# Performance work log

Measured on AMD Instinct MI355X. Metric: run time of the kernel, lower is better.

## Reference

```python
import jax, jax.numpy as jnp
import numpy as np

P = 8192  # num_particles
C = 8192  # num EEG channels (must equal P for the original broadcast to be valid)


def setup_inputs() -> dict:
    key = jax.random.key(0)
    k1, k2, k3, k4, k5 = jax.random.split(key, 5)
    inputs = jax.random.normal(k1, (1, C, P), dtype=jnp.float32)
    state_vector = jax.random.normal(k2, (P, 3), dtype=jnp.float32)
    # near-identity transition for numerical sanity
    transition_matrix = jnp.eye(3, dtype=jnp.float32) + 0.01 * jax.random.normal(k3, (3, 3), dtype=jnp.float32)
    # symmetric positive-definite process noise covariance (Cholesky must succeed)
    a = jax.random.normal(k4, (3, 3), dtype=jnp.float32)
    process_noise_cov = 0.01 * (a @ a.T) + 0.1 * jnp.eye(3, dtype=jnp.float32)
    forward_matrix = jax.random.normal(k5, (C, 3), dtype=jnp.float32)
    return {
        "inputs": inputs,
        "state_vector": state_vector,
        "transition_matrix": transition_matrix,
        "process_noise_cov": process_noise_cov,
        "forward_matrix": forward_matrix,
    }


def reference(inputs, state_vector, transition_matrix, process_noise_cov, forward_matrix):
    k_noise, k_cat = jax.random.split(jax.random.key(42))
    # --- state transition: x_new = x @ T^T + eps,  eps ~ N(0, Q) via z @ chol(Q) ---
    updated = state_vector @ transition_matrix.T                      # (P, 3)
    L = jnp.linalg.cholesky(process_noise_cov)                        # (3, 3) lower
    z = jax.random.normal(k_noise, (P, 3), dtype=state_vector.dtype)
    state = updated + z @ L                                           # (P, 3)
    # --- EEG measurement model: H @ x^T -> (C, P) ---
    predicted = forward_matrix @ state.T                              # (C, P)
    # --- particle weights: squared-residual sum (broadcast (1,C,P) - (P,C), C==P) ---
    w = jnp.sum(jnp.square(inputs - predicted.T), axis=-1)[0]         # (P,)
    # --- categorical resampling on log-weights (unnormalized logits) ---
    idx = jax.random.categorical(k_cat, jnp.log(w), shape=(P,))       # (P,) int
    resampled = state[idx]                                            # (P, 3) gather
    return jnp.mean(resampled, axis=0)                                # (3,)
```

## Files before the change

kernel.cpp:

```cpp
#include <hip/hip_runtime.h>
#include <stdint.h>

#define NP 8192
#define NC 8192

__host__ __device__ inline uint32_t rotl32(uint32_t x, int r) {
  return __builtin_rotateleft32(x, (unsigned)r);
}

__host__ __device__ inline void threefry2x32(uint32_t k0, uint32_t k1,
                                             uint32_t x0, uint32_t x1,
                                             uint32_t& o0, uint32_t& o1) {
  uint32_t ks2 = k0 ^ k1 ^ 0x1BD11BDAu;
  x0 += k0; x1 += k1;
#define TF_R(r) { x0 += x1; x1 = rotl32(x1, (r)); x1 ^= x0; }
  TF_R(13) TF_R(15) TF_R(26) TF_R(6)   x0 += k1;  x1 += ks2 + 1u;
  TF_R(17) TF_R(29) TF_R(16) TF_R(24)  x0 += ks2; x1 += k0 + 2u;
  TF_R(13) TF_R(15) TF_R(26) TF_R(6)   x0 += k0;  x1 += k1 + 3u;
  TF_R(17) TF_R(29) TF_R(16) TF_R(24)  x0 += k1;  x1 += ks2 + 4u;
  TF_R(13) TF_R(15) TF_R(26) TF_R(6)   x0 += ks2; x1 += k0 + 5u;
#undef TF_R
  o0 = x0; o1 = x1;
}

__device__ inline uint32_t tf_bits(uint32_t k0, uint32_t k1, uint32_t i) {
  uint32_t o0, o1;
  threefry2x32(k0, k1, 0u, i, o0, o1);
  return o0 ^ o1;
}

__device__ inline float u01(uint32_t bits) {
  return __uint_as_float((bits >> 9) | 0x3f800000u) - 1.0f;
}

__device__ inline float egen(uint32_t k0, uint32_t k1, uint32_t ctr) {
  const float TINY = 1.17549435e-38f;
  uint32_t bits = tf_bits(k0, k1, ctr);
  float v = fmaxf(u01(bits), TINY);
  return -__logf(v);
}

__device__ inline float erfinvf_(float x) {
  float w = -log1pf(-x * x);
  float p;
  if (w < 5.0f) {
    w -= 2.5f;
    p = 2.81022636e-08f;
    p = fmaf(p, w, 3.43273939e-07f);
    p = fmaf(p, w, -3.5233877e-06f);
    p = fmaf(p, w, -4.39150654e-06f);
    p = fmaf(p, w, 0.00021858087f);
    p = fmaf(p, w, -0.00125372503f);
    p = fmaf(p, w, -0.00417768164f);
    p = fmaf(p, w, 0.246640727f);
    p = fmaf(p, w, 1.50140941f);
  } else {
    w = sqrtf(w) - 3.0f;
    p = -0.000200214257f;
    p = fmaf(p, w, 0.000100950558f);
    p = fmaf(p, w, 0.00134934322f);
    p = fmaf(p, w, -0.00367342844f);
    p = fmaf(p, w, 0.00573950773f);
    p = fmaf(p, w, -0.0076224613f);
    p = fmaf(p, w, 0.00943887047f);
    p = fmaf(p, w, 1.00167406f);
    p = fmaf(p, w, 2.83297682f);
  }
  return p * x;
}

__global__ void __launch_bounds__(256) k_prep(uint32_t k0, uint32_t k1,
                                              const float* __restrict__ sv,
                                              const float* __restrict__ T,
                                              const float* __restrict__ Q,
                                              const float* __restrict__ H,
                                              float* __restrict__ st,
                                              float* __restrict__ ht) {
  int b = blockIdx.x;
  if (b < 32) {
    int i = b * 256 + threadIdx.x;
    const float lo = -0.99999994f;
    float zz[3];
#pragma unroll
    for (int k = 0; k < 3; k++) {
      uint32_t bits = tf_bits(k0, k1, 3u * (uint32_t)i + (uint32_t)k);
      float v = fmaxf(lo, u01(bits) * 2.0f + lo);
      zz[k] = 1.41421356f * erfinvf_(v);
    }
    float L00 = sqrtf(Q[0]);
    float L10 = Q[3] / L00, L20 = Q[6] / L00;
    float L11 = sqrtf(Q[4] - L10 * L10);
    float L21 = (Q[7] - L20 * L10) / L11;
    float L22 = sqrtf(Q[8] - L20 * L20 - L21 * L21);
    float s0 = sv[i * 3], s1 = sv[i * 3 + 1], s2 = sv[i * 3 + 2];
    float u0 = s0 * T[0] + s1 * T[1] + s2 * T[2];
    float u1 = s0 * T[3] + s1 * T[4] + s2 * T[5];
    float u2 = s0 * T[6] + s1 * T[7] + s2 * T[8];
    st[i * 3]     = u0 + (zz[0] * L00 + zz[1] * L10 + zz[2] * L20);
    st[i * 3 + 1] = u1 + (zz[1] * L11 + zz[2] * L21);
    st[i * 3 + 2] = u2 + (zz[2] * L22);
  } else {
    int t = (b - 32) * 256 + threadIdx.x;
    int k = t >> 13, j = t & (NP - 1);
    ht[t] = H[j * 3 + k];
  }
}

__global__ void __launch_bounds__(256) k_fused(uint32_t k0, uint32_t k1,
                                               const float* __restrict__ in,
                                               const float* __restrict__ ht,
                                               const float* __restrict__ st,
                                               float* __restrict__ winv,
                                               float* __restrict__ E) {
  int b = blockIdx.x;
  if (b % 5 == 0) {
    int w = b / 5;
    int wave = threadIdx.x >> 6;
    int lane = threadIdx.x & 63;
    int row = w * 4 + wave;
    float s0 = st[row * 3], s1 = st[row * 3 + 1], s2 = st[row * 3 + 2];
    const float4* inrow = (const float4*)(in + (size_t)row * NC);
    const float4* h0 = (const float4*)ht;
    const float4* h1 = (const float4*)(ht + NC);
    const float4* h2 = (const float4*)(ht + 2 * NC);
    float acc = 0.0f;
#pragma unroll 4
    for (int it = lane; it < NC / 4; it += 64) {
      float4 x = inrow[it];
      float4 a = h0[it];
      float4 bb = h1[it];
      float4 c = h2[it];
      float d0 = x.x - (a.x * s0 + bb.x * s1 + c.x * s2);
      float d1 = x.y - (a.y * s0 + bb.y * s1 + c.y * s2);
      float d2 = x.z - (a.z * s0 + bb.z * s1 + c.z * s2);
      float d3 = x.w - (a.w * s0 + bb.w * s1 + c.w * s2);
      acc += d0 * d0 + d1 * d1 + d2 * d2 + d3 * d3;
    }
#pragma unroll
    for (int off = 32; off > 0; off >>= 1) acc += __shfl_down(acc, off, 64);
    if (lane == 0) winv[row] = 1.0f / acc;
  } else {
    int s = b - b / 5 - 1;
    uint32_t base = (uint32_t)s * (uint32_t)NP;
    float4* erow = (float4*)(E + (size_t)s * NP);
#pragma unroll 2
    for (int p = 0; p < 8; ++p) {
      uint32_t i0 = (uint32_t)(p * 1024 + 4 * threadIdx.x);
      float4 e;
      e.x = egen(k0, k1, base + i0);
      e.y = egen(k0, k1, base + i0 + 1u);
      e.z = egen(k0, k1, base + i0 + 2u);
      e.w = egen(k0, k1, base + i0 + 3u);
      erow[i0 >> 2] = e;
    }
  }
}

__global__ void __launch_bounds__(256) k_race(const float* __restrict__ E,
                                              const float* __restrict__ winv,
                                              int* __restrict__ idx) {
  int wave = threadIdx.x >> 6;
  int lane = threadIdx.x & 63;
  int s = blockIdx.x * 4 + wave;
  const float4* erow = (const float4*)(E + (size_t)s * NP);
  const float4* wv = (const float4*)winv;
  float best = 3.4e38f;
  int bi = 0;
#pragma unroll 4
  for (int it = lane; it < NP / 4; it += 64) {
    float4 e = erow[it];
    float4 w = wv[it];
    int i = it * 4;
    float r0 = e.x * w.x;
    float r1 = e.y * w.y;
    float r2 = e.z * w.z;
    float r3 = e.w * w.w;
    if (r0 < best) { best = r0; bi = i; }
    if (r1 < best) { best = r1; bi = i + 1; }
    if (r2 < best) { best = r2; bi = i + 2; }
    if (r3 < best) { best = r3; bi = i + 3; }
  }
#pragma unroll
  for (int off = 32; off > 0; off >>= 1) {
    float ob = __shfl_down(best, off, 64);
    int oi = __shfl_down(bi, off, 64);
    if (ob < best || (ob == best && oi < bi)) { best = ob; bi = oi; }
  }
  if (lane == 0) idx[s] = bi;
}

__global__ void __launch_bounds__(256) k_weights(const float* __restrict__ in,
                                                 const float* __restrict__ ht,
                                                 const float* __restrict__ st,
                                                 float* __restrict__ winv) {
  int wave = threadIdx.x >> 6;
  int lane = threadIdx.x & 63;
  int row = blockIdx.x * 4 + wave;
  float s0 = st[row * 3], s1 = st[row * 3 + 1], s2 = st[row * 3 + 2];
  const float4* inrow = (const float4*)(in + (size_t)row * NC);
  const float4* h0 = (const float4*)ht;
  const float4* h1 = (const float4*)(ht + NC);
  const float4* h2 = (const float4*)(ht + 2 * NC);
  float acc = 0.0f;
#pragma unroll 4
  for (int it = lane; it < NC / 4; it += 64) {
    float4 x = inrow[it];
    float4 a = h0[it];
    float4 b = h1[it];
    float4 c = h2[it];
    float d0 = x.x - (a.x * s0 + b.x * s1 + c.x * s2);
    float d1 = x.y - (a.y * s0 + b.y * s1 + c.y * s2);
    float d2 = x.z - (a.z * s0 + b.z * s1 + c.z * s2);
    float d3 = x.w - (a.w * s0 + b.w * s1 + c.w * s2);
    acc += d0 * d0 + d1 * d1 + d2 * d2 + d3 * d3;
  }
#pragma unroll
  for (int off = 32; off > 0; off >>= 1) acc += __shfl_down(acc, off, 64);
  if (lane == 0) winv[row] = 1.0f / acc;
}

__global__ void __launch_bounds__(256) k_resample(uint32_t k0, uint32_t k1,
                                                  const float* __restrict__ winv,
                                                  int* __restrict__ idx) {
  uint32_t s = blockIdx.x;
  uint32_t base = s * (uint32_t)NP;
  const float TINY = 1.17549435e-38f;
  float best = 3.4e38f;
  int bi = 0;
#pragma unroll 4
  for (uint32_t i = threadIdx.x; i < NP; i += 256) {
    uint32_t bits = tf_bits(k0, k1, base + i);
    float v = fmaxf(u01(bits), TINY);
    float r = -__logf(v) * winv[i];
    if (r < best) { best = r; bi = (int)i; }
  }
  __shared__ float rv[256];
  __shared__ int ri[256];
  rv[threadIdx.x] = best;
  ri[threadIdx.x] = bi;
  __syncthreads();
  for (int stp = 128; stp > 0; stp >>= 1) {
    if (threadIdx.x < stp) {
      float va = rv[threadIdx.x], vb = rv[threadIdx.x + stp];
      int ia = ri[threadIdx.x], ib = ri[threadIdx.x + stp];
      if (vb < va || (vb == va && ib < ia)) { rv[threadIdx.x] = vb; ri[threadIdx.x] = ib; }
    }
    __syncthreads();
  }
  if (threadIdx.x == 0) idx[s] = ri[0];
}

__global__ void __launch_bounds__(1024) k_mean(const float* __restrict__ st,
                                               const int* __restrict__ idx,
                                               float* __restrict__ out) {
  double a0 = 0, a1 = 0, a2 = 0;
  for (int s = threadIdx.x; s < NP; s += 1024) {
    int j = idx[s];
    a0 += st[j * 3];
    a1 += st[j * 3 + 1];
    a2 += st[j * 3 + 2];
  }
  __shared__ double r0[1024], r1[1024], r2[1024];
  r0[threadIdx.x] = a0; r1[threadIdx.x] = a1; r2[threadIdx.x] = a2;
  __syncthreads();
  for (int s = 512; s > 0; s >>= 1) {
    if (threadIdx.x < s) {
      r0[threadIdx.x] += r0[threadIdx.x + s];
      r1[threadIdx.x] += r1[threadIdx.x + s];
      r2[threadIdx.x] += r2[threadIdx.x + s];
    }
    __syncthreads();
  }
  if (threadIdx.x == 0) {
    out[0] = (float)(r0[0] / NP);
    out[1] = (float)(r1[0] / NP);
    out[2] = (float)(r2[0] / NP);
  }
}

extern "C" void kernel_launch(void* const* d_in, const int* in_sizes, int n_in,
                              void* d_out, int out_size, void* d_ws, size_t ws_size,
                              hipStream_t stream) {
  const float* in = (const float*)d_in[0];
  const float* sv = (const float*)d_in[1];
  const float* T  = (const float*)d_in[2];
  const float* Q  = (const float*)d_in[3];
  const float* H  = (const float*)d_in[4];
  float* out = (float*)d_out;

  uint32_t nk0, nk1, ck0, ck1;
  threefry2x32(0u, 42u, 0u, 0u, nk0, nk1);
  threefry2x32(0u, 42u, 0u, 1u, ck0, ck1);

  const size_t eFloats = (size_t)NP * (size_t)NP;
  const size_t tailBytes = (24576 + 24576 + NP + NP) * 4;
  const bool fused = ws_size >= eFloats * 4 + tailBytes;

  if (fused) {
    float* E    = (float*)d_ws;
    float* st   = E + eFloats;
    float* ht   = st + 24576;
    float* winv = ht + 24576;
    int*   idx  = (int*)(winv + NP);

    hipLaunchKernelGGL(k_prep, dim3(128), dim3(256), 0, stream, nk0, nk1, sv, T, Q, H, st, ht);
    hipLaunchKernelGGL(k_fused, dim3(10240), dim3(256), 0, stream, ck0, ck1, in, ht, st, winv, E);
    hipLaunchKernelGGL(k_race, dim3(NP / 4), dim3(256), 0, stream, E, winv, idx);
    hipLaunchKernelGGL(k_mean, dim3(1), dim3(1024), 0, stream, st, idx, out);
  } else {
    float* st   = (float*)d_ws;
    float* ht   = st + 24576;
    float* winv = ht + 24576;
    int*   idx  = (int*)(winv + NP);

    hipLaunchKernelGGL(k_prep, dim3(128), dim3(256), 0, stream, nk0, nk1, sv, T, Q, H, st, ht);
    hipLaunchKernelGGL(k_weights, dim3(NP / 4), dim3(256), 0, stream, in, ht, st, winv);
    hipLaunchKernelGGL(k_resample, dim3(NP), dim3(256), 0, stream, ck0, ck1, winv, idx);
    hipLaunchKernelGGL(k_mean, dim3(1), dim3(1024), 0, stream, st, idx, out);
  }
}
```

Measured before the change: 527.9 us.

## Let noise blocks finish the resampling race early once all weights are ready

The fused kernel is rebalanced so weight blocks come first (two weight blocks per noise block in the first 3072 blocks). A global atomic counter records how many weight blocks have completed. A noise block that sees all weights done computes its argmin directly from registers and marks a flag, which skips writing its 256MB share of the E matrix. The race kernel then skips rows whose flag is set. This avoids E write and read traffic for late rows, at the cost of atomics, fences and extra register pressure from holding 32 noise values per thread.

```diff
diff --git a/kernel.cpp b/kernel.cpp
--- a/kernel.cpp
+++ b/kernel.cpp
@@ -3,6 +3,7 @@
 
 #define NP 8192
 #define NC 8192
+#define NWBLK 2048
 
 __host__ __device__ inline uint32_t rotl32(uint32_t x, int r) {
   return __builtin_rotateleft32(x, (unsigned)r);
@@ -75,7 +76,9 @@
                                               const float* __restrict__ Q,
                                               const float* __restrict__ H,
                                               float* __restrict__ st,
-                                              float* __restrict__ ht) {
+                                              float* __restrict__ ht,
+                                              int* __restrict__ flag,
+                                              int* __restrict__ ctrs) {
   int b = blockIdx.x;
   if (b < 32) {
     int i = b * 256 + threadIdx.x;
@@ -99,10 +102,14 @@
     st[i * 3]     = u0 + (zz[0] * L00 + zz[1] * L10 + zz[2] * L20);
     st[i * 3 + 1] = u1 + (zz[1] * L11 + zz[2] * L21);
     st[i * 3 + 2] = u2 + (zz[2] * L22);
-  } else {
+  } else if (b < 128) {
     int t = (b - 32) * 256 + threadIdx.x;
     int k = t >> 13, j = t & (NP - 1);
     ht[t] = H[j * 3 + k];
+  } else {
+    int t = (b - 128) * 256 + threadIdx.x;
+    flag[t] = 0;
+    if (b == 128 && threadIdx.x < 2) ctrs[threadIdx.x] = 0;
   }
 }
 
@@ -111,10 +118,14 @@
                                                const float* __restrict__ ht,
                                                const float* __restrict__ st,
                                                float* __restrict__ winv,
-                                               float* __restrict__ E) {
+                                               float* __restrict__ E,
+                                               int* __restrict__ flag,
+                                               int* __restrict__ idx,
+                                               int* __restrict__ ctrs) {
   int b = blockIdx.x;
-  if (b % 5 == 0) {
-    int w = b / 5;
+  bool isW = (b < 3072) && ((b % 3) < 2);
+  if (isW) {
+    int w = (b / 3) * 2 + (b % 3);
     int wave = threadIdx.x >> 6;
     int lane = threadIdx.x & 63;
     int row = w * 4 + wave;
@@ -139,29 +150,85 @@
 #pragma unroll
     for (int off = 32; off > 0; off >>= 1) acc += __shfl_down(acc, off, 64);
     if (lane == 0) winv[row] = 1.0f / acc;
+    __syncthreads();
+    if (threadIdx.x == 0) {
+      __threadfence();
+      __hip_atomic_fetch_add(&ctrs[0], 1, __ATOMIC_RELEASE, __HIP_MEMORY_SCOPE_AGENT);
+    }
   } else {
-    int s = b - b / 5 - 1;
+    int s = (b < 3072) ? (b / 3) : (1024 + (b - 3072));
     uint32_t base = (uint32_t)s * (uint32_t)NP;
-    float4* erow = (float4*)(E + (size_t)s * NP);
-#pragma unroll 2
+    float e[32];
+#pragma unroll
     for (int p = 0; p < 8; ++p) {
       uint32_t i0 = (uint32_t)(p * 1024 + 4 * threadIdx.x);
-      float4 e;
-      e.x = egen(k0, k1, base + i0);
-      e.y = egen(k0, k1, base + i0 + 1u);
-      e.z = egen(k0, k1, base + i0 + 2u);
-      e.w = egen(k0, k1, base + i0 + 3u);
-      erow[i0 >> 2] = e;
+      e[4 * p + 0] = egen(k0, k1, base + i0);
+      e[4 * p + 1] = egen(k0, k1, base + i0 + 1u);
+      e[4 * p + 2] = egen(k0, k1, base + i0 + 2u);
+      e[4 * p + 3] = egen(k0, k1, base + i0 + 3u);
+    }
+    __shared__ int rdy;
+    if (threadIdx.x == 0) {
+      rdy = (__hip_atomic_load(&ctrs[0], __ATOMIC_ACQUIRE,
+                               __HIP_MEMORY_SCOPE_AGENT) == NWBLK);
+    }
+    __syncthreads();
+    if (rdy) {
+      const float4* wv = (const float4*)winv;
+      float best = 3.4e38f;
+      int bi = 0;
+#pragma unroll
+      for (int p = 0; p < 8; ++p) {
+        uint32_t i0 = (uint32_t)(p * 1024 + 4 * threadIdx.x);
+        float4 w4 = wv[i0 >> 2];
+        float r0 = e[4 * p + 0] * w4.x;
+        float r1 = e[4 * p + 1] * w4.y;
+        float r2 = e[4 * p + 2] * w4.z;
+        float r3 = e[4 * p + 3] * w4.w;
+        int i = (int)i0;
+        if (r0 < best) { best = r0; bi = i; }
+        if (r1 < best) { best = r1; bi = i + 1; }
+        if (r2 < best) { best = r2; bi = i + 2; }
+        if (r3 < best) { best = r3; bi = i + 3; }
+      }
+      __shared__ float rv[256];
+      __shared__ int ri[256];
+      rv[threadIdx.x] = best;
+      ri[threadIdx.x] = bi;
+      __syncthreads();
+      for (int stp = 128; stp > 0; stp >>= 1) {
+        if (threadIdx.x < stp) {
+          float va = rv[threadIdx.x], vb = rv[threadIdx.x + stp];
+          int ia = ri[threadIdx.x], ib = ri[threadIdx.x + stp];
+          if (vb < va || (vb == va && ib < ia)) { rv[threadIdx.x] = vb; ri[threadIdx.x] = ib; }
+        }
+        __syncthreads();
+      }
+      if (threadIdx.x == 0) { idx[s] = ri[0]; flag[s] = 1; }
+    } else {
+      float4* erow = (float4*)(E + (size_t)s * NP);
+#pragma unroll
+      for (int p = 0; p < 8; ++p) {
+        uint32_t i0 = (uint32_t)(p * 1024 + 4 * threadIdx.x);
+        float4 e4;
+        e4.x = e[4 * p + 0];
+        e4.y = e[4 * p + 1];
+        e4.z = e[4 * p + 2];
+        e4.w = e[4 * p + 3];
+        erow[i0 >> 2] = e4;
+      }
     }
   }
 }
 
 __global__ void __launch_bounds__(256) k_race(const float* __restrict__ E,
                                               const float* __restrict__ winv,
+                                              const int* __restrict__ flag,
                                               int* __restrict__ idx) {
   int wave = threadIdx.x >> 6;
   int lane = threadIdx.x & 63;
   int s = blockIdx.x * 4 + wave;
+  if (flag[s]) return;
   const float4* erow = (const float4*)(E + (size_t)s * NP);
   const float4* wv = (const float4*)winv;
   float best = 3.4e38f;
@@ -187,6 +254,34 @@
     if (ob < best || (ob == best && oi < bi)) { best = ob; bi = oi; }
   }
   if (lane == 0) idx[s] = bi;
+}
+
+__global__ void __launch_bounds__(1024) k_mean(const float* __restrict__ st,
+                                               const int* __restrict__ idx,
+                                               float* __restrict__ out) {
+  double a0 = 0, a1 = 0, a2 = 0;
+  for (int s = threadIdx.x; s < NP; s += 1024) {
+    int j = idx[s];
+    a0 += st[j * 3];
+    a1 += st[j * 3 + 1];
+    a2 += st[j * 3 + 2];
+  }
+  __shared__ double r0[1024], r1[1024], r2[1024];
+  r0[threadIdx.x] = a0; r1[threadIdx.x] = a1; r2[threadIdx.x] = a2;
+  __syncthreads();
+  for (int s = 512; s > 0; s >>= 1) {
+    if (threadIdx.x < s) {
+      r0[threadIdx.x] += r0[threadIdx.x + s];
+      r1[threadIdx.x] += r1[threadIdx.x + s];
+      r2[threadIdx.x] += r2[threadIdx.x + s];
+    }
+    __syncthreads();
+  }
+  if (threadIdx.x == 0) {
+    out[0] = (float)(r0[0] / NP);
+    out[1] = (float)(r1[0] / NP);
+    out[2] = (float)(r2[0] / NP);
+  }
 }
 
 __global__ void __launch_bounds__(256) k_weights(const float* __restrict__ in,
@@ -250,34 +345,6 @@
   if (threadIdx.x == 0) idx[s] = ri[0];
 }
 
-__global__ void __launch_bounds__(1024) k_mean(const float* __restrict__ st,
-                                               const int* __restrict__ idx,
-                                               float* __restrict__ out) {
-  double a0 = 0, a1 = 0, a2 = 0;
-  for (int s = threadIdx.x; s < NP; s += 1024) {
-    int j = idx[s];
-    a0 += st[j * 3];
-    a1 += st[j * 3 + 1];
-    a2 += st[j * 3 + 2];
-  }
-  __shared__ double r0[1024], r1[1024], r2[1024];
-  r0[threadIdx.x] = a0; r1[threadIdx.x] = a1; r2[threadIdx.x] = a2;
-  __syncthreads();
-  for (int s = 512; s > 0; s >>= 1) {
-    if (threadIdx.x < s) {
-      r0[threadIdx.x] += r0[threadIdx.x + s];
-      r1[threadIdx.x] += r1[threadIdx.x + s];
-      r2[threadIdx.x] += r2[threadIdx.x + s];
-    }
-    __syncthreads();
-  }
-  if (threadIdx.x == 0) {
-    out[0] = (float)(r0[0] / NP);
-    out[1] = (float)(r1[0] / NP);
-    out[2] = (float)(r2[0] / NP);
-  }
-}
-
 extern "C" void kernel_launch(void* const* d_in, const int* in_sizes, int n_in,
                               void* d_out, int out_size, void* d_ws, size_t ws_size,
                               hipStream_t stream) {
@@ -293,7 +360,7 @@
   threefry2x32(0u, 42u, 0u, 1u, ck0, ck1);
 
   const size_t eFloats = (size_t)NP * (size_t)NP;
-  const size_t tailBytes = (24576 + 24576 + NP + NP) * 4;
+  const size_t tailBytes = (24576 + 24576 + NP + NP + NP + 2) * 4;
   const bool fused = ws_size >= eFloats * 4 + tailBytes;
 
   if (fused) {
@@ -302,10 +369,12 @@
     float* ht   = st + 24576;
     float* winv = ht + 24576;
     int*   idx  = (int*)(winv + NP);
-
-    hipLaunchKernelGGL(k_prep, dim3(128), dim3(256), 0, stream, nk0, nk1, sv, T, Q, H, st, ht);
-    hipLaunchKernelGGL(k_fused, dim3(10240), dim3(256), 0, stream, ck0, ck1, in, ht, st, winv, E);
-    hipLaunchKernelGGL(k_race, dim3(NP / 4), dim3(256), 0, stream, E, winv, idx);
+    int*   flag = idx + NP;
+    int*   ctrs = flag + NP;
+
+    hipLaunchKernelGGL(k_prep, dim3(160), dim3(256), 0, stream, nk0, nk1, sv, T, Q, H, st, ht, flag, ctrs);
+    hipLaunchKernelGGL(k_fused, dim3(10240), dim3(256), 0, stream, ck0, ck1, in, ht, st, winv, E, flag, idx, ctrs);
+    hipLaunchKernelGGL(k_race, dim3(NP / 4), dim3(256), 0, stream, E, winv, flag, idx);
     hipLaunchKernelGGL(k_mean, dim3(1), dim3(1024), 0, stream, st, idx, out);
   } else {
     float* st   = (float*)d_ws;
@@ -313,7 +382,7 @@
     float* winv = ht + 24576;
     int*   idx  = (int*)(winv + NP);
 
-    hipLaunchKernelGGL(k_prep, dim3(128), dim3(256), 0, stream, nk0, nk1, sv, T, Q, H, st, ht);
+    hipLaunchKernelGGL(k_prep, dim3(128), dim3(256), 0, stream, nk0, nk1, sv, T, Q, H, st, ht, (int*)nullptr, (int*)nullptr);
     hipLaunchKernelGGL(k_weights, dim3(NP / 4), dim3(256), 0, stream, in, ht, st, winv);
     hipLaunchKernelGGL(k_resample, dim3(NP), dim3(256), 0, stream, ck0, ck1, winv, idx);
     hipLaunchKernelGGL(k_mean, dim3(1), dim3(1024), 0, stream, st, idx, out);
```

Result: slower. 753.8 us (+42.8%).

## Split random-draw work between fused pass and race kernel

Applied to the files above, without the earlier changes.

The fused pass now precomputes only 6144 of the 8192 rows of categorical noise, interleaved with the weight computation in a 1:3 block pattern. The race kernel mixes blocks that scan stored noise rows with blocks that regenerate the remaining 2048 rows on the fly and race them against the weights. This rebalances RNG compute against the memory traffic of storing and reloading the noise matrix, so compute-bound and bandwidth-bound work overlap better. The cost is a more complex block mapping, and the on-the-fly blocks run heavier threefry and log work in the final pass.

```diff
diff --git a/kernel.cpp b/kernel.cpp
--- a/kernel.cpp
+++ b/kernel.cpp
@@ -3,6 +3,8 @@
 
 #define NP 8192
 #define NC 8192
+#define NS_E 6144
+#define NS_D 2048
 
 __host__ __device__ inline uint32_t rotl32(uint32_t x, int r) {
   return __builtin_rotateleft32(x, (unsigned)r);
@@ -113,8 +115,8 @@
                                                float* __restrict__ winv,
                                                float* __restrict__ E) {
   int b = blockIdx.x;
-  if (b % 5 == 0) {
-    int w = b / 5;
+  if ((b & 3) == 0) {
+    int w = b >> 2;
     int wave = threadIdx.x >> 6;
     int lane = threadIdx.x & 63;
     int row = w * 4 + wave;
@@ -140,7 +142,7 @@
     for (int off = 32; off > 0; off >>= 1) acc += __shfl_down(acc, off, 64);
     if (lane == 0) winv[row] = 1.0f / acc;
   } else {
-    int s = b - b / 5 - 1;
+    int s = b - (b >> 2) - 1;
     uint32_t base = (uint32_t)s * (uint32_t)NP;
     float4* erow = (float4*)(E + (size_t)s * NP);
 #pragma unroll 2
@@ -156,37 +158,98 @@
   }
 }
 
-__global__ void __launch_bounds__(256) k_race(const float* __restrict__ E,
+__global__ void __launch_bounds__(256) k_race(uint32_t k0, uint32_t k1,
+                                              const float* __restrict__ E,
                                               const float* __restrict__ winv,
                                               int* __restrict__ idx) {
-  int wave = threadIdx.x >> 6;
-  int lane = threadIdx.x & 63;
-  int s = blockIdx.x * 4 + wave;
-  const float4* erow = (const float4*)(E + (size_t)s * NP);
-  const float4* wv = (const float4*)winv;
-  float best = 3.4e38f;
-  int bi = 0;
-#pragma unroll 4
-  for (int it = lane; it < NP / 4; it += 64) {
-    float4 e = erow[it];
-    float4 w = wv[it];
-    int i = it * 4;
-    float r0 = e.x * w.x;
-    float r1 = e.y * w.y;
-    float r2 = e.z * w.z;
-    float r3 = e.w * w.w;
-    if (r0 < best) { best = r0; bi = i; }
-    if (r1 < best) { best = r1; bi = i + 1; }
-    if (r2 < best) { best = r2; bi = i + 2; }
-    if (r3 < best) { best = r3; bi = i + 3; }
-  }
+  int b = blockIdx.x;
+  int m = b % 7;
+  if (m < 3) {
+    int e = (b / 7) * 3 + m;
+    int wave = threadIdx.x >> 6;
+    int lane = threadIdx.x & 63;
+    int s = e * 4 + wave;
+    const float4* erow = (const float4*)(E + (size_t)s * NP);
+    const float4* wv = (const float4*)winv;
+    float best = 3.4e38f;
+    int bi = 0;
+#pragma unroll 4
+    for (int it = lane; it < NP / 4; it += 64) {
+      float4 ev = erow[it];
+      float4 w = wv[it];
+      int i = it * 4;
+      float r0 = ev.x * w.x;
+      float r1 = ev.y * w.y;
+      float r2 = ev.z * w.z;
+      float r3 = ev.w * w.w;
+      if (r0 < best) { best = r0; bi = i; }
+      if (r1 < best) { best = r1; bi = i + 1; }
+      if (r2 < best) { best = r2; bi = i + 2; }
+      if (r3 < best) { best = r3; bi = i + 3; }
+    }
 #pragma unroll
-  for (int off = 32; off > 0; off >>= 1) {
-    float ob = __shfl_down(best, off, 64);
-    int oi = __shfl_down(bi, off, 64);
-    if (ob < best || (ob == best && oi < bi)) { best = ob; bi = oi; }
-  }
-  if (lane == 0) idx[s] = bi;
+    for (int off = 32; off > 0; off >>= 1) {
+      float ob = __shfl_down(best, off, 64);
+      int oi = __shfl_down(bi, off, 64);
+      if (ob < best || (ob == best && oi < bi)) { best = ob; bi = oi; }
+    }
+    if (lane == 0) idx[s] = bi;
+  } else {
+    uint32_t s = (uint32_t)(NS_E + (b / 7) * 4 + (m - 3));
+    uint32_t base = s * (uint32_t)NP;
+    const float TINY = 1.17549435e-38f;
+    float best = 3.4e38f;
+    int bi = 0;
+#pragma unroll 4
+    for (uint32_t i = threadIdx.x; i < NP; i += 256) {
+      uint32_t bits = tf_bits(k0, k1, base + i);
+      float v = fmaxf(u01(bits), TINY);
+      float r = -__logf(v) * winv[i];
+      if (r < best) { best = r; bi = (int)i; }
+    }
+    __shared__ float rv[256];
+    __shared__ int ri[256];
+    rv[threadIdx.x] = best;
+    ri[threadIdx.x] = bi;
+    __syncthreads();
+    for (int stp = 128; stp > 0; stp >>= 1) {
+      if (threadIdx.x < stp) {
+        float va = rv[threadIdx.x], vb = rv[threadIdx.x + stp];
+        int ia = ri[threadIdx.x], ib = ri[threadIdx.x + stp];
+        if (vb < va || (vb == va && ib < ia)) { rv[threadIdx.x] = vb; ri[threadIdx.x] = ib; }
+      }
+      __syncthreads();
+    }
+    if (threadIdx.x == 0) idx[s] = ri[0];
+  }
+}
+
+__global__ void __launch_bounds__(1024) k_mean(const float* __restrict__ st,
+                                               const int* __restrict__ idx,
+                                               float* __restrict__ out) {
+  double a0 = 0, a1 = 0, a2 = 0;
+  for (int s = threadIdx.x; s < NP; s += 1024) {
+    int j = idx[s];
+    a0 += st[j * 3];
+    a1 += st[j * 3 + 1];
+    a2 += st[j * 3 + 2];
+  }
+  __shared__ double r0[1024], r1[1024], r2[1024];
+  r0[threadIdx.x] = a0; r1[threadIdx.x] = a1; r2[threadIdx.x] = a2;
+  __syncthreads();
+  for (int s = 512; s > 0; s >>= 1) {
+    if (threadIdx.x < s) {
+      r0[threadIdx.x] += r0[threadIdx.x + s];
+      r1[threadIdx.x] += r1[threadIdx.x + s];
+      r2[threadIdx.x] += r2[threadIdx.x + s];
+    }
+    __syncthreads();
+  }
+  if (threadIdx.x == 0) {
+    out[0] = (float)(r0[0] / NP);
+    out[1] = (float)(r1[0] / NP);
+    out[2] = (float)(r2[0] / NP);
+  }
 }
 
 __global__ void __launch_bounds__(256) k_weights(const float* __restrict__ in,
@@ -250,34 +313,6 @@
   if (threadIdx.x == 0) idx[s] = ri[0];
 }
 
-__global__ void __launch_bounds__(1024) k_mean(const float* __restrict__ st,
-                                               const int* __restrict__ idx,
-                                               float* __restrict__ out) {
-  double a0 = 0, a1 = 0, a2 = 0;
-  for (int s = threadIdx.x; s < NP; s += 1024) {
-    int j = idx[s];
-    a0 += st[j * 3];
-    a1 += st[j * 3 + 1];
-    a2 += st[j * 3 + 2];
-  }
-  __shared__ double r0[1024], r1[1024], r2[1024];
-  r0[threadIdx.x] = a0; r1[threadIdx.x] = a1; r2[threadIdx.x] = a2;
-  __syncthreads();
-  for (int s = 512; s > 0; s >>= 1) {
-    if (threadIdx.x < s) {
-      r0[threadIdx.x] += r0[threadIdx.x + s];
-      r1[threadIdx.x] += r1[threadIdx.x + s];
-      r2[threadIdx.x] += r2[threadIdx.x + s];
-    }
-    __syncthreads();
-  }
-  if (threadIdx.x == 0) {
-    out[0] = (float)(r0[0] / NP);
-    out[1] = (float)(r1[0] / NP);
-    out[2] = (float)(r2[0] / NP);
-  }
-}
-
 extern "C" void kernel_launch(void* const* d_in, const int* in_sizes, int n_in,
                               void* d_out, int out_size, void* d_ws, size_t ws_size,
                               hipStream_t stream) {
@@ -304,8 +339,8 @@
     int*   idx  = (int*)(winv + NP);
 
     hipLaunchKernelGGL(k_prep, dim3(128), dim3(256), 0, stream, nk0, nk1, sv, T, Q, H, st, ht);
-    hipLaunchKernelGGL(k_fused, dim3(10240), dim3(256), 0, stream, ck0, ck1, in, ht, st, winv, E);
-    hipLaunchKernelGGL(k_race, dim3(NP / 4), dim3(256), 0, stream, E, winv, idx);
+    hipLaunchKernelGGL(k_fused, dim3(8192), dim3(256), 0, stream, ck0, ck1, in, ht, st, winv, E);
+    hipLaunchKernelGGL(k_race, dim3(3584), dim3(256), 0, stream, ck0, ck1, E, winv, idx);
     hipLaunchKernelGGL(k_mean, dim3(1), dim3(1024), 0, stream, st, idx, out);
   } else {
     float* st   = (float*)d_ws;
```

Result: slower. 663.0 us (+25.6%).
